# Kernel optimization log

Measured on AMD Instinct MI355X. Metric: run time of the kernel, lower is better.

## Reference

```python
import jax, jax.numpy as jnp
import numpy as np
import math

B, C, H, W = 4, 256, 64, 64
NUM_HEADS = 4
GROUPS = 32
EPS = 1e-5


def setup_inputs() -> dict:
    key = jax.random.key(0)
    ks = jax.random.split(key, 7)
    x = jax.random.normal(ks[0], (B, C, H, W), dtype=jnp.float32)
    gn_w = jax.random.normal(ks[1], (C,), dtype=jnp.float32) * 0.02 + 1.0
    gn_b = jax.random.normal(ks[2], (C,), dtype=jnp.float32) * 0.02
    qkv_w = jax.random.normal(ks[3], (3 * C, C), dtype=jnp.float32) * (1.0 / math.sqrt(C))
    qkv_b = jax.random.normal(ks[4], (3 * C,), dtype=jnp.float32) * 0.02
    proj_w = jax.random.normal(ks[5], (C, C), dtype=jnp.float32) * (1.0 / math.sqrt(C))
    proj_b = jax.random.normal(ks[6], (C,), dtype=jnp.float32) * 0.02
    return {"x": x, "gn_w": gn_w, "gn_b": gn_b, "qkv_w": qkv_w,
            "qkv_b": qkv_b, "proj_w": proj_w, "proj_b": proj_b}


def reference(x, gn_w, gn_b, qkv_w, qkv_b, proj_w, proj_b):
    b, c, h, w = x.shape
    t = h * w
    xf = x.reshape(b, c, t)                       # [B, C, T]

    # GroupNorm(32, C) over (channels-in-group, T)
    xg = xf.reshape(b, GROUPS, c // GROUPS, t)
    mean = jnp.mean(xg, axis=(2, 3), keepdims=True)
    var = jnp.var(xg, axis=(2, 3), keepdims=True)
    xn = ((xg - mean) * jax.lax.rsqrt(var + EPS)).reshape(b, c, t)
    xn = xn * gn_w[None, :, None] + gn_b[None, :, None]

    # 1x1 conv QKV: [B, 3C, T]
    qkv = jnp.einsum('oc,bct->bot', qkv_w, xn) + qkv_b[None, :, None]

    nh = NUM_HEADS
    ch = c // nh
    q, k, v = jnp.split(qkv, 3, axis=1)           # each [B, H*ch, T]
    q = q.reshape(b * nh, ch, t)
    k = k.reshape(b * nh, ch, t)
    v = v.reshape(b * nh, ch, t)

    scale = 1.0 / math.sqrt(math.sqrt(ch))
    logits = jnp.einsum('bct,bcs->bts', q * scale, k * scale)   # [B*H, T, T]
    weight = jax.nn.softmax(logits.astype(jnp.float32), axis=-1).astype(logits.dtype)
    a = jnp.einsum('bts,bcs->bct', weight, v)     # [B*H, ch, T]
    a = a.reshape(b, c, t)

    hproj = jnp.einsum('oc,bct->bot', proj_w, a) + proj_b[None, :, None]
    return (xf + hproj).reshape(b, c, h, w)
```

## Files before the change

### kernel.cpp

```cpp
#include <hip/hip_runtime.h>
#include <cstdint>
#include <cstddef>

#define TT 4096
#define CCH 256

typedef __attribute__((ext_vector_type(8))) short short8;
typedef __attribute__((ext_vector_type(4))) float f32x4;

__device__ __forceinline__ float bf2f(unsigned int u){
  union { unsigned int i; float f; } v; v.i = u << 16; return v.f;
}
__device__ __forceinline__ unsigned short f2bf(float f){
  unsigned int x = __float_as_uint(f);
  x += 0x7fffu + ((x >> 16) & 1u);
  return (unsigned short)(x >> 16);
}
__device__ __forceinline__ unsigned short f2bf_t(float f){
  return (unsigned short)(__float_as_uint(f) >> 16);
}
__device__ __forceinline__ int sw(int row, int col){
  return (row << 6) + ((((col >> 3) ^ (row & 7)) << 3)) + (col & 7);
}
__device__ __forceinline__ float bfly_max16(float x){
  unsigned a = __float_as_uint(x), b = a;
  asm("v_permlane16_swap_b32 %0, %1" : "+v"(a), "+v"(b));
  return fmaxf(__uint_as_float(a), __uint_as_float(b));
}
__device__ __forceinline__ float bfly_max32(float x){
  unsigned a = __float_as_uint(x), b = a;
  asm("v_permlane32_swap_b32 %0, %1" : "+v"(a), "+v"(b));
  return fmaxf(__uint_as_float(a), __uint_as_float(b));
}
__device__ __forceinline__ unsigned cvt_pk_bf16(float lo, float hi){
  unsigned r;
  asm("v_cvt_pk_bf16_f32 %0, %1, %2" : "=v"(r) : "v"(lo), "v"(hi));
  return r;
}

__global__ __launch_bounds__(256)
void wconv_gn(const float* __restrict__ qkv_w, const float* __restrict__ proj_w,
              const float* __restrict__ x,
              unsigned short* __restrict__ wq_bf, unsigned short* __restrict__ wp_bf,
              float* __restrict__ stats){
  int bid = blockIdx.x, tid = threadIdx.x;
  if (bid < 256){
    const float* src = (bid < 192) ? qkv_w : proj_w;
    unsigned short* dst = (bid < 192) ? wq_bf : wp_bf;
    int i = (bid < 192 ? bid : bid - 192) * 256 + tid;
    float4 u = *(const float4*)(src + (size_t)i * 4);
    ushort4 r; r.x = f2bf(u.x); r.y = f2bf(u.y); r.z = f2bf(u.z); r.w = f2bf(u.w);
    *(ushort4*)(dst + (size_t)i * 4) = r;
    return;
  }
  int sg = bid - 256;
  const float4* p = (const float4*)(x + (size_t)sg * 32768);
  float s = 0.f, sq = 0.f;
  #pragma unroll
  for (int it = 0; it < 32; ++it){
    float4 u = p[it * 256 + tid];
    s  += u.x + u.y + u.z + u.w;
    sq += u.x*u.x + u.y*u.y + u.z*u.z + u.w*u.w;
  }
  #pragma unroll
  for (int off = 32; off >= 1; off >>= 1){
    s  += __shfl_down(s, off);
    sq += __shfl_down(sq, off);
  }
  __shared__ float ls[4], lq[4];
  int w_ = tid >> 6, lane = tid & 63;
  if (lane == 0){ ls[w_] = s; lq[w_] = sq; }
  __syncthreads();
  if (tid == 0){
    float S = ls[0]+ls[1]+ls[2]+ls[3];
    float Q = lq[0]+lq[1]+lq[2]+lq[3];
    float mean = S * (1.f/32768.f);
    float var  = Q * (1.f/32768.f) - mean*mean;
    stats[2*sg]   = mean;
    stats[2*sg+1] = rsqrtf(var + 1e-5f);
  }
}

__global__ __launch_bounds__(256)
void gn_apply_t(const float* __restrict__ x, const float* __restrict__ gw,
                const float* __restrict__ gb, const float* __restrict__ stats,
                unsigned short* __restrict__ xnT){
  __shared__ unsigned short t_lds[64][72];
  int tid = threadIdx.x;
  int t0 = blockIdx.x << 6, c0 = blockIdx.y << 6, b = blockIdx.z;
  int t4 = (tid & 15) << 2, cr = tid >> 4;
  #pragma unroll
  for (int pass = 0; pass < 4; ++pass){
    int cl = (pass << 4) + cr;
    int c = c0 + cl;
    int sg = (b << 5) | (c >> 3);
    float mean = stats[2*sg], rstd = stats[2*sg+1];
    float sc = gw[c] * rstd;
    float sh = gb[c] - mean * sc;
    float4 u = *(const float4*)(x + ((size_t)(b*CCH + c))*TT + t0 + t4);
    t_lds[t4+0][cl] = f2bf(u.x*sc + sh);
    t_lds[t4+1][cl] = f2bf(u.y*sc + sh);
    t_lds[t4+2][cl] = f2bf(u.z*sc + sh);
    t_lds[t4+3][cl] = f2bf(u.w*sc + sh);
  }
  __syncthreads();
  #pragma unroll
  for (int pass = 0; pass < 2; ++pass){
    int chunk = (pass << 8) + tid;
    int row = chunk >> 3, c8 = (chunk & 7) << 3;
    *(uint4*)(xnT + ((size_t)b*TT + t0 + row)*256 + c0 + c8) = *(const uint4*)&t_lds[row][c8];
  }
}

__global__ __launch_bounds__(256)
void qkv_mfma(const unsigned short* __restrict__ wb, const float* __restrict__ bias,
              const unsigned short* __restrict__ xnT,
              unsigned short* __restrict__ qT, unsigned short* __restrict__ kT,
              unsigned short* __restrict__ vO){
  __shared__ unsigned short x_lds[4096];
  int tid = threadIdx.x;
  int w = tid >> 6, lane = tid & 63, quad = lane >> 4, l15 = lane & 15;
  int t0 = blockIdx.x << 6, o0 = blockIdx.y << 6, b = blockIdx.z;
  const unsigned short* xb = xnT + (size_t)b * TT * 256;
  const unsigned short* wrow = wb + (size_t)(o0 + (w << 4) + l15) * 256;
  f32x4 acc[4];
  #pragma unroll
  for (int nt = 0; nt < 4; ++nt) acc[nt] = (f32x4){0.f,0.f,0.f,0.f};
  for (int ks = 0; ks < 4; ++ks){
    int k0 = ks << 6;
    __syncthreads();
    #pragma unroll
    for (int pass = 0; pass < 2; ++pass){
      int chunk = (pass << 8) + tid;
      int row = chunk >> 3, c8 = (chunk & 7) << 3;
      *(uint4*)&x_lds[sw(row, c8)] = *(const uint4*)(xb + (size_t)(t0 + row)*256 + k0 + c8);
    }
    __syncthreads();
    short8 wa0 = *(const short8*)(wrow + k0 + (quad << 3));
    short8 wa1 = *(const short8*)(wrow + k0 + 32 + (quad << 3));
    #pragma unroll
    for (int nt = 0; nt < 4; ++nt){
      short8 xb0 = *(const short8*)&x_lds[sw((nt << 4) + l15, quad << 3)];
      short8 xb1 = *(const short8*)&x_lds[sw((nt << 4) + l15, 32 + (quad << 3))];
      acc[nt] = __builtin_amdgcn_mfma_f32_16x16x32_bf16(wa0, xb0, acc[nt], 0, 0, 0);
      acc[nt] = __builtin_amdgcn_mfma_f32_16x16x32_bf16(wa1, xb1, acc[nt], 0, 0, 0);
    }
  }
  int sec = blockIdx.y >> 2, h = blockIdx.y & 3, bh = (b << 2) | h;
  float bs[4];
  #pragma unroll
  for (int r = 0; r < 4; ++r) bs[r] = bias[o0 + (w << 4) + (quad << 2) + r];
  __syncthreads();
  if (sec < 2){
    float qsc = (sec == 0) ? 0.125f * 1.44269504f : 1.0f;
    #pragma unroll
    for (int nt = 0; nt < 4; ++nt){
      ushort4 pk;
      pk.x = f2bf((acc[nt][0] + bs[0]) * qsc);
      pk.y = f2bf((acc[nt][1] + bs[1]) * qsc);
      pk.z = f2bf((acc[nt][2] + bs[2]) * qsc);
      pk.w = f2bf((acc[nt][3] + bs[3]) * qsc);
      *(ushort4*)&x_lds[sw((nt << 4) + l15, (w << 4) + (quad << 2))] = pk;
    }
    __syncthreads();
    unsigned short* dst = (sec == 0) ? qT : kT;
    #pragma unroll
    for (int pass = 0; pass < 2; ++pass){
      int chunk = (pass << 8) + tid;
      int row = chunk >> 3, c8 = (chunk & 7) << 3;
      *(uint4*)(dst + ((size_t)bh*TT + t0 + row)*64 + c8) = *(const uint4*)&x_lds[sw(row, c8)];
    }
  } else {
    #pragma unroll
    for (int nt = 0; nt < 4; ++nt)
      #pragma unroll
      for (int r = 0; r < 4; ++r)
        x_lds[sw((w << 4) + (quad << 2) + r, (nt << 4) + l15)] = f2bf(acc[nt][r] + bs[r]);
    __syncthreads();
    #pragma unroll
    for (int pass = 0; pass < 2; ++pass){
      int chunk = (pass << 8) + tid;
      int row = chunk >> 3, c8 = (chunk & 7) << 3;
      *(uint4*)(vO + ((size_t)bh*64 + row)*TT + t0 + c8) = *(const uint4*)&x_lds[sw(row, c8)];
    }
  }
}

__global__ __launch_bounds__(256, 4)
void attn7(const unsigned short* __restrict__ qT, const unsigned short* __restrict__ kT,
           const unsigned short* __restrict__ vO, unsigned short* __restrict__ aT){
  __shared__ __align__(16) unsigned short k_lds[4096];
  __shared__ __align__(16) unsigned short v_lds[4096];
  __shared__ __align__(16) unsigned short p_lds[4096];
  int tid = threadIdx.x;
  int w = tid >> 6, lane = tid & 63, quad = lane >> 4, l15 = lane & 15;
  int bh = blockIdx.x & 15, qt6 = blockIdx.x >> 4;
  int t0 = qt6 << 6;
  const unsigned short* qg = qT + (size_t)bh * TT * 64;
  const unsigned short* kg = kT + (size_t)bh * TT * 64;
  const unsigned short* vg = vO + (size_t)bh * 64 * TT;
  int tw = t0 + (w << 4);

  int row0 = tid >> 3, c80 = (tid & 7) << 3;
  int row1 = row0 + 32;
  int soff0 = sw(row0, c80), soff1 = sw(row1, c80);

  short8 qf[2];
  qf[0] = *(const short8*)(qg + (size_t)(tw + l15)*64 + (quad << 3));
  qf[1] = *(const short8*)(qg + (size_t)(tw + l15)*64 + 32 + (quad << 3));

  short8 ones;
  #pragma unroll
  for (int i = 0; i < 8; ++i) ones[i] = (short)0x3F80;

  f32x4 o_acc[4];
  #pragma unroll
  for (int ct = 0; ct < 4; ++ct) o_acc[ct] = (f32x4){0.f,0.f,0.f,0.f};
  float m_ = -1e30f, l_ = 0.f;

  uint4 kr0 = *(const uint4*)(kg + (size_t)row0*64 + c80);
  uint4 kr1 = *(const uint4*)(kg + (size_t)row1*64 + c80);
  uint4 vr0 = *(const uint4*)(vg + (size_t)row0*TT + c80);
  uint4 vr1 = *(const uint4*)(vg + (size_t)row1*TT + c80);

  int prow = (w << 4) + l15;

  for (int st = 0; st < 64; ++st){
    __syncthreads();
    *(uint4*)&k_lds[soff0] = kr0;
    *(uint4*)&k_lds[soff1] = kr1;
    *(uint4*)&v_lds[soff0] = vr0;
    *(uint4*)&v_lds[soff1] = vr1;
    if (st < 63){
      int sn = (st + 1) << 6;
      kr0 = *(const uint4*)(kg + (size_t)(sn + row0)*64 + c80);
      kr1 = *(const uint4*)(kg + (size_t)(sn + row1)*64 + c80);
      vr0 = *(const uint4*)(vg + (size_t)row0*TT + sn + c80);
      vr1 = *(const uint4*)(vg + (size_t)row1*TT + sn + c80);
    }
    __syncthreads();
    f32x4 sv[4];
    __builtin_amdgcn_s_setprio(1);
    #pragma unroll
    for (int mt = 0; mt < 4; ++mt){
      short8 ka0 = *(const short8*)&k_lds[sw((mt << 4) + l15, quad << 3)];
      short8 ka1 = *(const short8*)&k_lds[sw((mt << 4) + l15, 32 + (quad << 3))];
      f32x4 z = (f32x4){0.f,0.f,0.f,0.f};
      z = __builtin_amdgcn_mfma_f32_16x16x32_bf16(ka0, qf[0], z, 0, 0, 0);
      z = __builtin_amdgcn_mfma_f32_16x16x32_bf16(ka1, qf[1], z, 0, 0, 0);
      sv[mt] = z;
    }
    __builtin_amdgcn_s_setprio(0);
    float rm = fmaxf(fmaxf(sv[0][0], sv[0][1]), fmaxf(sv[0][2], sv[0][3]));
    #pragma unroll
    for (int mt = 1; mt < 4; ++mt)
      rm = fmaxf(rm, fmaxf(fmaxf(sv[mt][0], sv[mt][1]), fmaxf(sv[mt][2], sv[mt][3])));
    rm = bfly_max16(rm);
    rm = bfly_max32(rm);
    float alpha = 1.0f;
    if (__ballot(rm > m_ + 8.0f)){
      float mnew = fmaxf(m_, rm);
      alpha = exp2f(m_ - mnew);
      m_ = mnew;
      #pragma unroll
      for (int ct = 0; ct < 4; ++ct)
        #pragma unroll
        for (int r = 0; r < 4; ++r) o_acc[ct][r] *= alpha;
    }
    #pragma unroll
    for (int mt = 0; mt < 4; ++mt){
      float p0 = exp2f(sv[mt][0] - m_);
      float p1 = exp2f(sv[mt][1] - m_);
      float p2 = exp2f(sv[mt][2] - m_);
      float p3 = exp2f(sv[mt][3] - m_);
      uint2 pkk;
      pkk.x = cvt_pk_bf16(p0, p1);
      pkk.y = cvt_pk_bf16(p2, p3);
      *(uint2*)&p_lds[sw(prow, (mt << 4) + (quad << 2))] = pkk;
    }
    short8 pb0 = *(const short8*)&p_lds[sw(prow, quad << 3)];
    short8 pb1 = *(const short8*)&p_lds[sw(prow, 32 + (quad << 3))];
    __builtin_amdgcn_s_setprio(1);
    f32x4 ls4 = (f32x4){0.f,0.f,0.f,0.f};
    ls4 = __builtin_amdgcn_mfma_f32_16x16x32_bf16(ones, pb0, ls4, 0, 0, 0);
    ls4 = __builtin_amdgcn_mfma_f32_16x16x32_bf16(ones, pb1, ls4, 0, 0, 0);
    #pragma unroll
    for (int ct = 0; ct < 4; ++ct){
      short8 va0 = *(const short8*)&v_lds[sw((ct << 4) + l15, quad << 3)];
      short8 va1 = *(const short8*)&v_lds[sw((ct << 4) + l15, 32 + (quad << 3))];
      o_acc[ct] = __builtin_amdgcn_mfma_f32_16x16x32_bf16(va0, pb0, o_acc[ct], 0, 0, 0);
      o_acc[ct] = __builtin_amdgcn_mfma_f32_16x16x32_bf16(va1, pb1, o_acc[ct], 0, 0, 0);
    }
    __builtin_amdgcn_s_setprio(0);
    l_ = l_ * alpha + ls4[0];
  }
  __syncthreads();
  float ir = 1.f / l_;
  #pragma unroll
  for (int ct = 0; ct < 4; ++ct){
    ushort4 ok;
    ok.x = f2bf(o_acc[ct][0] * ir);
    ok.y = f2bf(o_acc[ct][1] * ir);
    ok.z = f2bf(o_acc[ct][2] * ir);
    ok.w = f2bf(o_acc[ct][3] * ir);
    *(ushort4*)&p_lds[sw(prow, (ct << 4) + (quad << 2))] = ok;
  }
  __syncthreads();
  size_t abase = ((size_t)(bh >> 2)*TT + t0)*256 + (size_t)(bh & 3)*64;
  #pragma unroll
  for (int pass = 0; pass < 2; ++pass){
    int chunk = (pass << 8) + tid;
    int row = chunk >> 3, c8 = (chunk & 7) << 3;
    *(uint4*)(aT + abase + (size_t)row*256 + c8) = *(const uint4*)&p_lds[sw(row, c8)];
  }
}

__global__ __launch_bounds__(256)
void proj_mfma(const unsigned short* __restrict__ wb, const float* __restrict__ bias,
               const unsigned short* __restrict__ aT, const float* __restrict__ x,
               float* __restrict__ out){
  __shared__ unsigned short x_lds[4096];
  int tid = threadIdx.x;
  int w = tid >> 6, lane = tid & 63, quad = lane >> 4, l15 = lane & 15;
  int t0 = blockIdx.x << 6, o0 = blockIdx.y << 6, b = blockIdx.z;
  const unsigned short* xb = aT + (size_t)b * TT * 256;
  const unsigned short* wrow = wb + (size_t)(o0 + (w << 4) + l15) * 256;
  f32x4 acc[4];
  #pragma unroll
  for (int nt = 0; nt < 4; ++nt) acc[nt] = (f32x4){0.f,0.f,0.f,0.f};
  for (int ks = 0; ks < 4; ++ks){
    int k0 = ks << 6;
    __syncthreads();
    #pragma unroll
    for (int pass = 0; pass < 2; ++pass){
      int chunk = (pass << 8) + tid;
      int row = chunk >> 3, c8 = (chunk & 7) << 3;
      *(uint4*)&x_lds[sw(row, c8)] = *(const uint4*)(xb + (size_t)(t0 + row)*256 + k0 + c8);
    }
    __syncthreads();
    short8 wa0 = *(const short8*)(wrow + k0 + (quad << 3));
    short8 wa1 = *(const short8*)(wrow + k0 + 32 + (quad << 3));
    #pragma unroll
    for (int nt = 0; nt < 4; ++nt){
      short8 xb0 = *(const short8*)&x_lds[sw((nt << 4) + l15, quad << 3)];
      short8 xb1 = *(const short8*)&x_lds[sw((nt << 4) + l15, 32 + (quad << 3))];
      acc[nt] = __builtin_amdgcn_mfma_f32_16x16x32_bf16(wa0, xb0, acc[nt], 0, 0, 0);
      acc[nt] = __builtin_amdgcn_mfma_f32_16x16x32_bf16(wa1, xb1, acc[nt], 0, 0, 0);
    }
  }
  #pragma unroll
  for (int r = 0; r < 4; ++r){
    int o = o0 + (w << 4) + (quad << 2) + r;
    float bsv = bias[o];
    #pragma unroll
    for (int nt = 0; nt < 4; ++nt){
      size_t idx = ((size_t)(b*CCH + o))*TT + t0 + (nt << 4) + l15;
      out[idx] = acc[nt][r] + bsv + x[idx];
    }
  }
}

extern "C" void kernel_launch(void* const* d_in, const int* in_sizes, int n_in,
                              void* d_out, int out_size, void* d_ws, size_t ws_size,
                              hipStream_t stream){
  const float* x      = (const float*)d_in[0];
  const float* gn_w   = (const float*)d_in[1];
  const float* gn_b   = (const float*)d_in[2];
  const float* qkv_w  = (const float*)d_in[3];
  const float* qkv_b  = (const float*)d_in[4];
  const float* proj_w = (const float*)d_in[5];
  const float* proj_b = (const float*)d_in[6];
  float* out = (float*)d_out;

  float* stats = (float*)d_ws;
  unsigned short* wq_bf = (unsigned short*)(stats + 1024);
  unsigned short* wp_bf = wq_bf + (size_t)768*256;
  unsigned short* xnT   = wp_bf + (size_t)256*256;
  unsigned short* qT    = xnT + (size_t)4*TT*256;
  unsigned short* kT    = qT  + (size_t)16*TT*64;
  unsigned short* vO    = kT  + (size_t)16*TT*64;
  unsigned short* aT    = vO  + (size_t)16*64*TT;

  wconv_gn<<<384, 256, 0, stream>>>(qkv_w, proj_w, x, wq_bf, wp_bf, stats);
  gn_apply_t<<<dim3(64, 4, 4), 256, 0, stream>>>(x, gn_w, gn_b, stats, xnT);
  qkv_mfma<<<dim3(64, 12, 4), 256, 0, stream>>>(wq_bf, qkv_b, xnT, qT, kT, vO);
  attn7<<<1024, 256, 0, stream>>>(qT, kT, vO, aT);
  proj_mfma<<<dim3(64, 4, 4), 256, 0, stream>>>(wp_bf, proj_b, aT, x, out);
}
```

Baseline: 239.3 us.

## Process two query tiles per attention block to reuse K/V tiles

The attention kernel now handles 128 query rows per block (two 64-row subtiles per wave), so each K/V tile loaded into LDS feeds twice as many MFMAs. The grid is halved to 512 blocks and the occupancy hint drops from 4 to 2 blocks per CU to fit the extra accumulators. The lazy rescale (ballot with threshold) is replaced by an unconditional rescale each step, and the P conversion uses software rounding instead of v_cvt_pk_bf16. This adds register pressure and lowers parallelism, with 512 blocks on 256 CUs, in exchange for halving the K/V global loads and LDS staging.

Result: slower. 261.0 us (+9.1%).

```diff
diff --git a/kernel.cpp b/kernel.cpp
--- a/kernel.cpp
+++ b/kernel.cpp
@@ -8,34 +8,29 @@
 typedef __attribute__((ext_vector_type(8))) short short8;
 typedef __attribute__((ext_vector_type(4))) float f32x4;
 
-__device__ __forceinline__ float bf2f(unsigned int u){
-  union { unsigned int i; float f; } v; v.i = u << 16; return v.f;
-}
 __device__ __forceinline__ unsigned short f2bf(float f){
   unsigned int x = __float_as_uint(f);
   x += 0x7fffu + ((x >> 16) & 1u);
   return (unsigned short)(x >> 16);
 }
-__device__ __forceinline__ unsigned short f2bf_t(float f){
-  return (unsigned short)(__float_as_uint(f) >> 16);
-}
 __device__ __forceinline__ int sw(int row, int col){
   return (row << 6) + ((((col >> 3) ^ (row & 7)) << 3)) + (col & 7);
 }
+__device__ __forceinline__ void pl16(unsigned &a, unsigned &b){
+  asm("v_permlane16_swap_b32 %0, %1" : "+v"(a), "+v"(b));
+}
+__device__ __forceinline__ void pl32(unsigned &a, unsigned &b){
+  asm("v_permlane32_swap_b32 %0, %1" : "+v"(a), "+v"(b));
+}
 __device__ __forceinline__ float bfly_max16(float x){
   unsigned a = __float_as_uint(x), b = a;
-  asm("v_permlane16_swap_b32 %0, %1" : "+v"(a), "+v"(b));
+  pl16(a, b);
   return fmaxf(__uint_as_float(a), __uint_as_float(b));
 }
 __device__ __forceinline__ float bfly_max32(float x){
   unsigned a = __float_as_uint(x), b = a;
-  asm("v_permlane32_swap_b32 %0, %1" : "+v"(a), "+v"(b));
+  pl32(a, b);
   return fmaxf(__uint_as_float(a), __uint_as_float(b));
-}
-__device__ __forceinline__ unsigned cvt_pk_bf16(float lo, float hi){
-  unsigned r;
-  asm("v_cvt_pk_bf16_f32 %0, %1, %2" : "=v"(r) : "v"(lo), "v"(hi));
-  return r;
 }
 
 __global__ __launch_bounds__(256)
@@ -186,44 +181,45 @@
   }
 }
 
-__global__ __launch_bounds__(256, 4)
-void attn7(const unsigned short* __restrict__ qT, const unsigned short* __restrict__ kT,
+__global__ __launch_bounds__(256, 2)
+void attn9(const unsigned short* __restrict__ qT, const unsigned short* __restrict__ kT,
            const unsigned short* __restrict__ vO, unsigned short* __restrict__ aT){
   __shared__ __align__(16) unsigned short k_lds[4096];
   __shared__ __align__(16) unsigned short v_lds[4096];
-  __shared__ __align__(16) unsigned short p_lds[4096];
+  __shared__ __align__(16) unsigned short p_lds[8192];
   int tid = threadIdx.x;
   int w = tid >> 6, lane = tid & 63, quad = lane >> 4, l15 = lane & 15;
-  int bh = blockIdx.x & 15, qt6 = blockIdx.x >> 4;
-  int t0 = qt6 << 6;
+  int bh = blockIdx.x & 15, t0 = (blockIdx.x >> 4) << 7;
   const unsigned short* qg = qT + (size_t)bh * TT * 64;
   const unsigned short* kg = kT + (size_t)bh * TT * 64;
   const unsigned short* vg = vO + (size_t)bh * 64 * TT;
-  int tw = t0 + (w << 4);
 
   int row0 = tid >> 3, c80 = (tid & 7) << 3;
   int row1 = row0 + 32;
   int soff0 = sw(row0, c80), soff1 = sw(row1, c80);
 
-  short8 qf[2];
-  qf[0] = *(const short8*)(qg + (size_t)(tw + l15)*64 + (quad << 3));
-  qf[1] = *(const short8*)(qg + (size_t)(tw + l15)*64 + 32 + (quad << 3));
+  short8 qf[2][2];
+  #pragma unroll
+  for (int tt2 = 0; tt2 < 2; ++tt2)
+    #pragma unroll
+    for (int h = 0; h < 2; ++h)
+      qf[tt2][h] = *(const short8*)(qg + (size_t)(t0 + (tt2<<6) + (w<<4) + l15)*64 + (h<<5) + (quad<<3));
 
   short8 ones;
   #pragma unroll
   for (int i = 0; i < 8; ++i) ones[i] = (short)0x3F80;
 
-  f32x4 o_acc[4];
-  #pragma unroll
-  for (int ct = 0; ct < 4; ++ct) o_acc[ct] = (f32x4){0.f,0.f,0.f,0.f};
-  float m_ = -1e30f, l_ = 0.f;
+  f32x4 o_acc[2][4];
+  #pragma unroll
+  for (int tt2 = 0; tt2 < 2; ++tt2)
+    #pragma unroll
+    for (int ct = 0; ct < 4; ++ct) o_acc[tt2][ct] = (f32x4){0.f,0.f,0.f,0.f};
+  float m_[2] = {-1e30f, -1e30f}, l_[2] = {0.f, 0.f};
 
   uint4 kr0 = *(const uint4*)(kg + (size_t)row0*64 + c80);
   uint4 kr1 = *(const uint4*)(kg + (size_t)row1*64 + c80);
   uint4 vr0 = *(const uint4*)(vg + (size_t)row0*TT + c80);
   uint4 vr1 = *(const uint4*)(vg + (size_t)row1*TT + c80);
-
-  int prow = (w << 4) + l15;
 
   for (int st = 0; st < 64; ++st){
     __syncthreads();
@@ -239,76 +235,90 @@
       vr1 = *(const uint4*)(vg + (size_t)row1*TT + sn + c80);
     }
     __syncthreads();
-    f32x4 sv[4];
+    f32x4 sv[2][4];
     __builtin_amdgcn_s_setprio(1);
     #pragma unroll
     for (int mt = 0; mt < 4; ++mt){
       short8 ka0 = *(const short8*)&k_lds[sw((mt << 4) + l15, quad << 3)];
       short8 ka1 = *(const short8*)&k_lds[sw((mt << 4) + l15, 32 + (quad << 3))];
-      f32x4 z = (f32x4){0.f,0.f,0.f,0.f};
-      z = __builtin_amdgcn_mfma_f32_16x16x32_bf16(ka0, qf[0], z, 0, 0, 0);
-      z = __builtin_amdgcn_mfma_f32_16x16x32_bf16(ka1, qf[1], z, 0, 0, 0);
-      sv[mt] = z;
+      #pragma unroll
+      for (int tt2 = 0; tt2 < 2; ++tt2){
+        f32x4 z = (f32x4){0.f,0.f,0.f,0.f};
+        z = __builtin_amdgcn_mfma_f32_16x16x32_bf16(ka0, qf[tt2][0], z, 0, 0, 0);
+        z = __builtin_amdgcn_mfma_f32_16x16x32_bf16(ka1, qf[tt2][1], z, 0, 0, 0);
+        sv[tt2][mt] = z;
+      }
     }
     __builtin_amdgcn_s_setprio(0);
-    float rm = fmaxf(fmaxf(sv[0][0], sv[0][1]), fmaxf(sv[0][2], sv[0][3]));
-    #pragma unroll
-    for (int mt = 1; mt < 4; ++mt)
-      rm = fmaxf(rm, fmaxf(fmaxf(sv[mt][0], sv[mt][1]), fmaxf(sv[mt][2], sv[mt][3])));
-    rm = bfly_max16(rm);
-    rm = bfly_max32(rm);
-    float alpha = 1.0f;
-    if (__ballot(rm > m_ + 8.0f)){
-      float mnew = fmaxf(m_, rm);
-      alpha = exp2f(m_ - mnew);
-      m_ = mnew;
+    short8 pb[2][2];
+    float alpha[2];
+    #pragma unroll
+    for (int tt2 = 0; tt2 < 2; ++tt2){
+      float rm = fmaxf(fmaxf(sv[tt2][0][0], sv[tt2][0][1]), fmaxf(sv[tt2][0][2], sv[tt2][0][3]));
+      #pragma unroll
+      for (int mt = 1; mt < 4; ++mt)
+        rm = fmaxf(rm, fmaxf(fmaxf(sv[tt2][mt][0], sv[tt2][mt][1]),
+                             fmaxf(sv[tt2][mt][2], sv[tt2][mt][3])));
+      rm = bfly_max16(rm);
+      rm = bfly_max32(rm);
+      float mnew = fmaxf(m_[tt2], rm);
+      alpha[tt2] = exp2f(m_[tt2] - mnew);
+      m_[tt2] = mnew;
       #pragma unroll
       for (int ct = 0; ct < 4; ++ct)
         #pragma unroll
-        for (int r = 0; r < 4; ++r) o_acc[ct][r] *= alpha;
-    }
-    #pragma unroll
-    for (int mt = 0; mt < 4; ++mt){
-      float p0 = exp2f(sv[mt][0] - m_);
-      float p1 = exp2f(sv[mt][1] - m_);
-      float p2 = exp2f(sv[mt][2] - m_);
-      float p3 = exp2f(sv[mt][3] - m_);
-      uint2 pkk;
-      pkk.x = cvt_pk_bf16(p0, p1);
-      pkk.y = cvt_pk_bf16(p2, p3);
-      *(uint2*)&p_lds[sw(prow, (mt << 4) + (quad << 2))] = pkk;
-    }
-    short8 pb0 = *(const short8*)&p_lds[sw(prow, quad << 3)];
-    short8 pb1 = *(const short8*)&p_lds[sw(prow, 32 + (quad << 3))];
+        for (int r = 0; r < 4; ++r) o_acc[tt2][ct][r] *= alpha[tt2];
+      int prow = (tt2 << 6) + (w << 4) + l15;
+      #pragma unroll
+      for (int mt = 0; mt < 4; ++mt){
+        ushort4 pk;
+        pk.x = f2bf(exp2f(sv[tt2][mt][0] - m_[tt2]));
+        pk.y = f2bf(exp2f(sv[tt2][mt][1] - m_[tt2]));
+        pk.z = f2bf(exp2f(sv[tt2][mt][2] - m_[tt2]));
+        pk.w = f2bf(exp2f(sv[tt2][mt][3] - m_[tt2]));
+        *(ushort4*)&p_lds[sw(prow, (mt << 4) + (quad << 2))] = pk;
+      }
+      asm volatile("" ::: "memory");
+      __builtin_amdgcn_sched_barrier(0);
+      pb[tt2][0] = *(const short8*)&p_lds[sw(prow, quad << 3)];
+      pb[tt2][1] = *(const short8*)&p_lds[sw(prow, 32 + (quad << 3))];
+      f32x4 ls4 = (f32x4){0.f,0.f,0.f,0.f};
+      ls4 = __builtin_amdgcn_mfma_f32_16x16x32_bf16(ones, pb[tt2][0], ls4, 0, 0, 0);
+      ls4 = __builtin_amdgcn_mfma_f32_16x16x32_bf16(ones, pb[tt2][1], ls4, 0, 0, 0);
+      l_[tt2] = l_[tt2] * alpha[tt2] + ls4[0];
+    }
     __builtin_amdgcn_s_setprio(1);
-    f32x4 ls4 = (f32x4){0.f,0.f,0.f,0.f};
-    ls4 = __builtin_amdgcn_mfma_f32_16x16x32_bf16(ones, pb0, ls4, 0, 0, 0);
-    ls4 = __builtin_amdgcn_mfma_f32_16x16x32_bf16(ones, pb1, ls4, 0, 0, 0);
     #pragma unroll
     for (int ct = 0; ct < 4; ++ct){
       short8 va0 = *(const short8*)&v_lds[sw((ct << 4) + l15, quad << 3)];
       short8 va1 = *(const short8*)&v_lds[sw((ct << 4) + l15, 32 + (quad << 3))];
-      o_acc[ct] = __builtin_amdgcn_mfma_f32_16x16x32_bf16(va0, pb0, o_acc[ct], 0, 0, 0);
-      o_acc[ct] = __builtin_amdgcn_mfma_f32_16x16x32_bf16(va1, pb1, o_acc[ct], 0, 0, 0);
+      #pragma unroll
+      for (int tt2 = 0; tt2 < 2; ++tt2){
+        o_acc[tt2][ct] = __builtin_amdgcn_mfma_f32_16x16x32_bf16(va0, pb[tt2][0], o_acc[tt2][ct], 0, 0, 0);
+        o_acc[tt2][ct] = __builtin_amdgcn_mfma_f32_16x16x32_bf16(va1, pb[tt2][1], o_acc[tt2][ct], 0, 0, 0);
+      }
     }
     __builtin_amdgcn_s_setprio(0);
-    l_ = l_ * alpha + ls4[0];
-  }
-  __syncthreads();
-  float ir = 1.f / l_;
-  #pragma unroll
-  for (int ct = 0; ct < 4; ++ct){
-    ushort4 ok;
-    ok.x = f2bf(o_acc[ct][0] * ir);
-    ok.y = f2bf(o_acc[ct][1] * ir);
-    ok.z = f2bf(o_acc[ct][2] * ir);
-    ok.w = f2bf(o_acc[ct][3] * ir);
-    *(ushort4*)&p_lds[sw(prow, (ct << 4) + (quad << 2))] = ok;
+  }
+  __syncthreads();
+  #pragma unroll
+  for (int tt2 = 0; tt2 < 2; ++tt2){
+    float ir = 1.f / l_[tt2];
+    int prow = (tt2 << 6) + (w << 4) + l15;
+    #pragma unroll
+    for (int ct = 0; ct < 4; ++ct){
+      ushort4 ok;
+      ok.x = f2bf(o_acc[tt2][ct][0] * ir);
+      ok.y = f2bf(o_acc[tt2][ct][1] * ir);
+      ok.z = f2bf(o_acc[tt2][ct][2] * ir);
+      ok.w = f2bf(o_acc[tt2][ct][3] * ir);
+      *(ushort4*)&p_lds[sw(prow, (ct << 4) + (quad << 2))] = ok;
+    }
   }
   __syncthreads();
   size_t abase = ((size_t)(bh >> 2)*TT + t0)*256 + (size_t)(bh & 3)*64;
   #pragma unroll
-  for (int pass = 0; pass < 2; ++pass){
+  for (int pass = 0; pass < 4; ++pass){
     int chunk = (pass << 8) + tid;
     int row = chunk >> 3, c8 = (chunk & 7) << 3;
     *(uint4*)(aT + abase + (size_t)row*256 + c8) = *(const uint4*)&p_lds[sw(row, c8)];
@@ -384,6 +394,6 @@
   wconv_gn<<<384, 256, 0, stream>>>(qkv_w, proj_w, x, wq_bf, wp_bf, stats);
   gn_apply_t<<<dim3(64, 4, 4), 256, 0, stream>>>(x, gn_w, gn_b, stats, xnT);
   qkv_mfma<<<dim3(64, 12, 4), 256, 0, stream>>>(wq_bf, qkv_b, xnT, qT, kT, vO);
-  attn7<<<1024, 256, 0, stream>>>(qT, kT, vO, aT);
+  attn9<<<512, 256, 0, stream>>>(qT, kT, vO, aT);
   proj_mfma<<<dim3(64, 4, 4), 256, 0, stream>>>(wp_bf, proj_b, aT, x, out);
 }
```

## Double-buffer K/V tiles in LDS with one barrier per iteration

Applied to the files above, without the earlier changes.

The attention kernel now keeps two LDS buffers for K and V. It writes the next tile into the alternate buffer while computing on the current one, and prefetches global data two tiles ahead. This cuts the loop from two __syncthreads to one per step, removing a barrier stall. In exchange, LDS use per block grows from about 24 KB to 40 KB, which may lower occupancy below the requested 4 blocks per CU. A sched_barrier is also added around the P write/read.

Result: no change. 242.5 us (+1.3%).

```diff
diff --git a/kernel.cpp b/kernel.cpp
--- a/kernel.cpp
+++ b/kernel.cpp
@@ -8,9 +8,6 @@
 typedef __attribute__((ext_vector_type(8))) short short8;
 typedef __attribute__((ext_vector_type(4))) float f32x4;
 
-__device__ __forceinline__ float bf2f(unsigned int u){
-  union { unsigned int i; float f; } v; v.i = u << 16; return v.f;
-}
 __device__ __forceinline__ unsigned short f2bf(float f){
   unsigned int x = __float_as_uint(f);
   x += 0x7fffu + ((x >> 16) & 1u);
@@ -22,14 +19,20 @@
 __device__ __forceinline__ int sw(int row, int col){
   return (row << 6) + ((((col >> 3) ^ (row & 7)) << 3)) + (col & 7);
 }
+__device__ __forceinline__ void pl16(unsigned &a, unsigned &b){
+  asm("v_permlane16_swap_b32 %0, %1" : "+v"(a), "+v"(b));
+}
+__device__ __forceinline__ void pl32(unsigned &a, unsigned &b){
+  asm("v_permlane32_swap_b32 %0, %1" : "+v"(a), "+v"(b));
+}
 __device__ __forceinline__ float bfly_max16(float x){
   unsigned a = __float_as_uint(x), b = a;
-  asm("v_permlane16_swap_b32 %0, %1" : "+v"(a), "+v"(b));
+  pl16(a, b);
   return fmaxf(__uint_as_float(a), __uint_as_float(b));
 }
 __device__ __forceinline__ float bfly_max32(float x){
   unsigned a = __float_as_uint(x), b = a;
-  asm("v_permlane32_swap_b32 %0, %1" : "+v"(a), "+v"(b));
+  pl32(a, b);
   return fmaxf(__uint_as_float(a), __uint_as_float(b));
 }
 __device__ __forceinline__ unsigned cvt_pk_bf16(float lo, float hi){
@@ -189,8 +192,8 @@
 __global__ __launch_bounds__(256, 4)
 void attn7(const unsigned short* __restrict__ qT, const unsigned short* __restrict__ kT,
            const unsigned short* __restrict__ vO, unsigned short* __restrict__ aT){
-  __shared__ __align__(16) unsigned short k_lds[4096];
-  __shared__ __align__(16) unsigned short v_lds[4096];
+  __shared__ __align__(16) unsigned short k_lds[8192];
+  __shared__ __align__(16) unsigned short v_lds[8192];
   __shared__ __align__(16) unsigned short p_lds[4096];
   int tid = threadIdx.x;
   int w = tid >> 6, lane = tid & 63, quad = lane >> 4, l15 = lane & 15;
@@ -222,29 +225,39 @@
   uint4 kr1 = *(const uint4*)(kg + (size_t)row1*64 + c80);
   uint4 vr0 = *(const uint4*)(vg + (size_t)row0*TT + c80);
   uint4 vr1 = *(const uint4*)(vg + (size_t)row1*TT + c80);
+  *(uint4*)&k_lds[soff0] = kr0;
+  *(uint4*)&k_lds[soff1] = kr1;
+  *(uint4*)&v_lds[soff0] = vr0;
+  *(uint4*)&v_lds[soff1] = vr1;
+  kr0 = *(const uint4*)(kg + (size_t)(64 + row0)*64 + c80);
+  kr1 = *(const uint4*)(kg + (size_t)(64 + row1)*64 + c80);
+  vr0 = *(const uint4*)(vg + (size_t)row0*TT + 64 + c80);
+  vr1 = *(const uint4*)(vg + (size_t)row1*TT + 64 + c80);
+  __syncthreads();
 
   int prow = (w << 4) + l15;
-
   for (int st = 0; st < 64; ++st){
-    __syncthreads();
-    *(uint4*)&k_lds[soff0] = kr0;
-    *(uint4*)&k_lds[soff1] = kr1;
-    *(uint4*)&v_lds[soff0] = vr0;
-    *(uint4*)&v_lds[soff1] = vr1;
+    int cur = (st & 1) << 12;
+    int nxt = ((st + 1) & 1) << 12;
     if (st < 63){
-      int sn = (st + 1) << 6;
+      *(uint4*)&k_lds[nxt + soff0] = kr0;
+      *(uint4*)&k_lds[nxt + soff1] = kr1;
+      *(uint4*)&v_lds[nxt + soff0] = vr0;
+      *(uint4*)&v_lds[nxt + soff1] = vr1;
+    }
+    if (st < 62){
+      int sn = (st + 2) << 6;
       kr0 = *(const uint4*)(kg + (size_t)(sn + row0)*64 + c80);
       kr1 = *(const uint4*)(kg + (size_t)(sn + row1)*64 + c80);
       vr0 = *(const uint4*)(vg + (size_t)row0*TT + sn + c80);
       vr1 = *(const uint4*)(vg + (size_t)row1*TT + sn + c80);
     }
-    __syncthreads();
     f32x4 sv[4];
     __builtin_amdgcn_s_setprio(1);
     #pragma unroll
     for (int mt = 0; mt < 4; ++mt){
-      short8 ka0 = *(const short8*)&k_lds[sw((mt << 4) + l15, quad << 3)];
-      short8 ka1 = *(const short8*)&k_lds[sw((mt << 4) + l15, 32 + (quad << 3))];
+      short8 ka0 = *(const short8*)&k_lds[cur + sw((mt << 4) + l15, quad << 3)];
+      short8 ka1 = *(const short8*)&k_lds[cur + sw((mt << 4) + l15, 32 + (quad << 3))];
       f32x4 z = (f32x4){0.f,0.f,0.f,0.f};
       z = __builtin_amdgcn_mfma_f32_16x16x32_bf16(ka0, qf[0], z, 0, 0, 0);
       z = __builtin_amdgcn_mfma_f32_16x16x32_bf16(ka1, qf[1], z, 0, 0, 0);
@@ -278,6 +291,8 @@
       pkk.y = cvt_pk_bf16(p2, p3);
       *(uint2*)&p_lds[sw(prow, (mt << 4) + (quad << 2))] = pkk;
     }
+    asm volatile("" ::: "memory");
+    __builtin_amdgcn_sched_barrier(0);
     short8 pb0 = *(const short8*)&p_lds[sw(prow, quad << 3)];
     short8 pb1 = *(const short8*)&p_lds[sw(prow, 32 + (quad << 3))];
     __builtin_amdgcn_s_setprio(1);
@@ -286,15 +301,15 @@
     ls4 = __builtin_amdgcn_mfma_f32_16x16x32_bf16(ones, pb1, ls4, 0, 0, 0);
     #pragma unroll
     for (int ct = 0; ct < 4; ++ct){
-      short8 va0 = *(const short8*)&v_lds[sw((ct << 4) + l15, quad << 3)];
-      short8 va1 = *(const short8*)&v_lds[sw((ct << 4) + l15, 32 + (quad << 3))];
+      short8 va0 = *(const short8*)&v_lds[cur + sw((ct << 4) + l15, quad << 3)];
+      short8 va1 = *(const short8*)&v_lds[cur + sw((ct << 4) + l15, 32 + (quad << 3))];
       o_acc[ct] = __builtin_amdgcn_mfma_f32_16x16x32_bf16(va0, pb0, o_acc[ct], 0, 0, 0);
       o_acc[ct] = __builtin_amdgcn_mfma_f32_16x16x32_bf16(va1, pb1, o_acc[ct], 0, 0, 0);
     }
     __builtin_amdgcn_s_setprio(0);
     l_ = l_ * alpha + ls4[0];
-  }
-  __syncthreads();
+    __syncthreads();
+  }
   float ir = 1.f / l_;
   #pragma unroll
   for (int ct = 0; ct < 4; ++ct){
```
